# Performance work log

Hardware: AMD Instinct MI355X
Metric: run time of the kernel (lower is better)

The kernel has to match this reference:

```python
import math
import jax, jax.numpy as jnp
import numpy as np

G, NP, L = 256, 24, 3            # graphs, atoms per graph, GPS layers
C, TDIM, NFREQ, NT = 256, 256, 10, 100
EDIM = NFREQ * 2 * 3 + 9         # SinusoidsEmbedding.dim + lattice_input_dim = 69
N = G * NP                       # 6144 nodes
H = 4                            # attention heads


def _silu(x):
    return x * jax.nn.sigmoid(x)


def _bn(x, g, b):
    # BatchNorm1d, training-mode batch statistics (biased var), eps=1e-5
    m = x.mean(0)
    v = ((x - m) ** 2).mean(0)
    return (x - m) * jax.lax.rsqrt(v + 1e-5) * g + b


def _forward(t, frac_coords, lattice, type_emb, node_align_W, node_align_b,
             gine_edge_W, gine_edge_b, gine_W1, gine_b1, gine_W2, gine_b2,
             attn_in_W, attn_in_b, attn_out_W, attn_out_b,
             mlp_W1, mlp_b1, mlp_W2, mlp_b2,
             bn1_g, bn1_b, bn2_g, bn2_b, bn3_g, bn3_b, ln_g, ln_b,
             tro_W1, tro_b1, tro_W2, tro_b2,
             lat_W1, lat_b1, lat_W2, lat_b2, lat_W3,
             fc_W1, fc_b1, fc_W2, fc_b2, fc_W3,
             atom_types, node2graph, edge_src, edge_dst):
    # sinusoidal time embedding [G, TDIM], repeated per node
    half = TDIM // 2
    tf = jnp.exp(jnp.arange(half, dtype=jnp.float32) * (-math.log(10000.0) / (half - 1)))
    te = t[:, None] * tf[None, :]
    te = jnp.concatenate([jnp.sin(te), jnp.cos(te)], -1)
    time_emb = jnp.repeat(te, NP, axis=0)                      # [N, TDIM]
    x = jnp.concatenate([type_emb[atom_types], time_emb], 1) @ node_align_W + node_align_b

    # edge features: sinusoids of periodic frac diff + per-graph lattice
    fd = (frac_coords[edge_dst] - frac_coords[edge_src]) % 1.0  # [E,3]
    sf = 2.0 * math.pi * jnp.arange(NFREQ, dtype=jnp.float32)
    emb = (fd[..., None] * sf).reshape(-1, 3 * NFREQ)
    eattr = jnp.concatenate([jnp.sin(emb), jnp.cos(emb), lattice[node2graph[edge_src]]], 1)

    scale = 1.0 / math.sqrt(C // H)
    for l in range(L):
        # --- GINEConv: gather -> relu(x_j + edge_emb) -> scatter-add -> MLP ---
        eemb = eattr @ gine_edge_W[l] + gine_edge_b[l]          # [E, C]
        msg = jax.nn.relu(x[edge_src] + eemb)
        aggr = jax.ops.segment_sum(msg, edge_dst, num_segments=N)
        z = x + aggr                                            # (1+eps)*x, eps=0
        z = _silu(z @ gine_W1[l] + gine_b1[l]) @ gine_W2[l] + gine_b2[l]
        h1 = _bn(z + x, bn1_g[l], bn1_b[l])
        # --- dense-batched multihead self-attention (all graphs have NP nodes) ---
        xd = x.reshape(G, NP, C)
        qkv = xd @ attn_in_W[l] + attn_in_b[l]
        q, k, v = jnp.split(qkv, 3, axis=-1)
        q = q.reshape(G, NP, H, C // H).transpose(0, 2, 1, 3)
        k = k.reshape(G, NP, H, C // H).transpose(0, 2, 1, 3)
        v = v.reshape(G, NP, H, C // H).transpose(0, 2, 1, 3)
        a = jax.nn.softmax(jnp.einsum('ghqd,ghkd->ghqk', q, k) * scale, axis=-1)
        o = jnp.einsum('ghqk,ghkd->ghqd', a, v).transpose(0, 2, 1, 3).reshape(G, NP, C)
        o = (o @ attn_out_W[l] + attn_out_b[l]).reshape(N, C)
        h2 = _bn(o + x, bn2_g[l], bn2_b[l])
        # --- combine + MLP (GPSConv default: ReLU, dropout=0) ---
        out = h1 + h2
        out = out + jax.nn.relu(out @ mlp_W1[l] + mlp_b1[l]) @ mlp_W2[l] + mlp_b2[l]
        x = _bn(out, bn3_g[l], bn3_b[l])

    # final LayerNorm over feature dim
    m = x.mean(-1, keepdims=True)
    v = ((x - m) ** 2).mean(-1, keepdims=True)
    hn = (x - m) * jax.lax.rsqrt(v + 1e-5) * ln_g + ln_b

    # scatter-mean graph pooling
    cnt = jax.ops.segment_sum(jnp.ones((N, 1), hn.dtype), node2graph, num_segments=G)
    gf = jax.ops.segment_sum(hn, node2graph, num_segments=G) / cnt

    types_pred = _silu(hn @ tro_W1 + tro_b1) @ tro_W2 + tro_b2
    lattice_pred = _silu(_silu(gf @ lat_W1 + lat_b1) @ lat_W2 + lat_b2) @ lat_W3
    frac_pred = _silu(_silu(hn @ fc_W1 + fc_b1) @ fc_W2 + fc_b2) @ fc_W3
    return types_pred, lattice_pred, frac_pred


def setup_inputs() -> dict:
    key = jax.random.key(0)
    ki = iter(jax.random.split(key, 40))

    def nrm(shape, s=0.02):
        return jax.random.normal(next(ki), shape, jnp.float32) * s

    # block-diagonal fully-connected edges, dense_to_sparse row-major order
    g = np.repeat(np.arange(G), NP * NP)
    i = np.tile(np.repeat(np.arange(NP), NP), G)
    j = np.tile(np.tile(np.arange(NP), NP), G)
    inp = {
        "t": jax.random.uniform(next(ki), (G,), jnp.float32),
        "frac_coords": jax.random.uniform(next(ki), (N, 3), jnp.float32),
        "lattice": nrm((G, 9), 1.0),
        "type_emb": nrm((NT, C)),
        "node_align_W": nrm((C + TDIM, C)), "node_align_b": jnp.zeros((C,), jnp.float32),
        "gine_edge_W": nrm((L, EDIM, C)), "gine_edge_b": jnp.zeros((L, C), jnp.float32),
        "gine_W1": nrm((L, C, C)), "gine_b1": jnp.zeros((L, C), jnp.float32),
        "gine_W2": nrm((L, C, C)), "gine_b2": jnp.zeros((L, C), jnp.float32),
        "attn_in_W": nrm((L, C, 3 * C)), "attn_in_b": jnp.zeros((L, 3 * C), jnp.float32),
        "attn_out_W": nrm((L, C, C)), "attn_out_b": jnp.zeros((L, C), jnp.float32),
        "mlp_W1": nrm((L, C, 2 * C)), "mlp_b1": jnp.zeros((L, 2 * C), jnp.float32),
        "mlp_W2": nrm((L, 2 * C, C)), "mlp_b2": jnp.zeros((L, C), jnp.float32),
        "bn1_g": jnp.ones((L, C), jnp.float32), "bn1_b": jnp.zeros((L, C), jnp.float32),
        "bn2_g": jnp.ones((L, C), jnp.float32), "bn2_b": jnp.zeros((L, C), jnp.float32),
        "bn3_g": jnp.ones((L, C), jnp.float32), "bn3_b": jnp.zeros((L, C), jnp.float32),
        "ln_g": jnp.ones((C,), jnp.float32), "ln_b": jnp.zeros((C,), jnp.float32),
        "tro_W1": nrm((C, C // 2)), "tro_b1": jnp.zeros((C // 2,), jnp.float32),
        "tro_W2": nrm((C // 2, NT)), "tro_b2": jnp.zeros((NT,), jnp.float32),
        "lat_W1": nrm((C, C // 2)), "lat_b1": jnp.zeros((C // 2,), jnp.float32),
        "lat_W2": nrm((C // 2, C // 4)), "lat_b2": jnp.zeros((C // 4,), jnp.float32),
        "lat_W3": nrm((C // 4, 9)),
        "fc_W1": nrm((C, C // 2)), "fc_b1": jnp.zeros((C // 2,), jnp.float32),
        "fc_W2": nrm((C // 2, C // 4)), "fc_b2": jnp.zeros((C // 4,), jnp.float32),
        "fc_W3": nrm((C // 4, 3)),
        "atom_types": jax.random.randint(next(ki), (N,), 0, NT, jnp.int32),
        "node2graph": jnp.asarray(np.repeat(np.arange(G), NP), jnp.int32),
        "edge_src": jnp.asarray(g * NP + i, jnp.int32),
        "edge_dst": jnp.asarray(g * NP + j, jnp.int32),
    }
    return inp


def reference(t, frac_coords, lattice, type_emb, node_align_W, node_align_b,
              gine_edge_W, gine_edge_b, gine_W1, gine_b1, gine_W2, gine_b2,
              attn_in_W, attn_in_b, attn_out_W, attn_out_b,
              mlp_W1, mlp_b1, mlp_W2, mlp_b2,
              bn1_g, bn1_b, bn2_g, bn2_b, bn3_g, bn3_b, ln_g, ln_b,
              tro_W1, tro_b1, tro_W2, tro_b2,
              lat_W1, lat_b1, lat_W2, lat_b2, lat_W3,
              fc_W1, fc_b1, fc_W2, fc_b2, fc_W3,
              atom_types, node2graph, edge_src, edge_dst):
    return _forward(t, frac_coords, lattice, type_emb, node_align_W, node_align_b,
                    gine_edge_W, gine_edge_b, gine_W1, gine_b1, gine_W2, gine_b2,
                    attn_in_W, attn_in_b, attn_out_W, attn_out_b,
                    mlp_W1, mlp_b1, mlp_W2, mlp_b2,
                    bn1_g, bn1_b, bn2_g, bn2_b, bn3_g, bn3_b, ln_g, ln_b,
                    tro_W1, tro_b1, tro_W2, tro_b2,
                    lat_W1, lat_b1, lat_W2, lat_b2, lat_W3,
                    fc_W1, fc_b1, fc_W2, fc_b2, fc_W3,
                    atom_types, node2graph, edge_src, edge_dst)
```

## Files before the change

kernel.cpp:

```cpp
#include <hip/hip_runtime.h>
#include <hip/hip_bf16.h>
#include <math.h>

#define GG 256
#define NP 24
#define LL 3
#define CC 256
#define NN (GG*NP)
#define HH 4
#define DH 64

typedef __hip_bfloat16 bf;
typedef __attribute__((ext_vector_type(8))) short bfrag;
typedef __attribute__((ext_vector_type(4))) float ffrag;

__device__ __forceinline__ short pk(float x) {
    union { bf h; short s; } u; u.h = __float2bfloat16(x); return u.s;
}
__device__ __forceinline__ float b2f_s(short x) {
    union { short s; bf h; } u; u.s = x; return __bfloat162float(u.h);
}

typedef __attribute__((address_space(1))) const void gv_t;
typedef __attribute__((address_space(3))) void lv_t;

__global__ void detect_int_k(const unsigned int* __restrict__ at, int* flags) {
    __shared__ int ok;
    if (threadIdx.x == 0) ok = 1;
    __syncthreads();
    if (at[2 * threadIdx.x + 1] != 0u) ok = 0;
    __syncthreads();
    if (threadIdx.x == 0) flags[0] = ok;
}

__global__ void signal_k(float* out, int n, float val) {
    int i = blockIdx.x * 256 + threadIdx.x;
    if (i < n) out[i] = val;
}

struct TArgs {
    const float* src[9];
    long dstOff[9];
    int K[9], N[9], L[9];
    int blk0[10];
};
__global__ void transp_all(TArgs a, bf* __restrict__ wt) {
    int bid = blockIdx.x;
    int s = 0;
    while (s < 8 && bid >= a.blk0[s + 1]) ++s;
    long idx = (long)(bid - a.blk0[s]) * 256 + threadIdx.x;
    int KN = a.K[s] * a.N[s];
    long sz = (long)KN * a.L[s];
    if (idx >= sz) return;
    int l = (int)(idx / KN);
    int rem = (int)(idx % KN);
    int k = rem / a.N[s], n = rem % a.N[s];
    wt[a.dstOff[s] + (long)l * KN + (long)n * a.K[s] + k] =
        __float2bfloat16(a.src[s][idx]);
}

#define ETAB_ELEMS (GG * 24 * 24 * 64)
__global__ void prep_gewtab(const float* __restrict__ geW, short* __restrict__ wh,
                            short* __restrict__ wl, const float* __restrict__ frac,
                            short* __restrict__ eh, short* __restrict__ el) {
    int bid = blockIdx.x;
    if (bid < 192) {
        int idx = bid * 256 + threadIdx.x;
        if (idx >= 49152) return;
        int k = idx & 63;
        int n = (idx >> 6) & 127;
        int half = (idx >> 13) & 1;
        int l = idx >> 14;
        float v = (k < 60) ? geW[(long)l * 69 * 256 + (long)k * 256 + half * 128 + n] : 0.f;
        short hi = pk(v);
        short lo = pk(v - b2f_s(hi));
        wh[idx] = hi;
        wl[idx] = lo;
    } else {
        int idx = (bid - 192) * 256 + threadIdx.x;
        if (idx >= ETAB_ELEMS) return;
        int k = idx & 63;
        int rem = idx >> 6;
        int i = rem % 24;
        int rem2 = rem / 24;
        int j = rem2 % 24;
        int g = rem2 / 24;
        float val = 0.f;
        if (k < 60) {
            int r = (k < 30) ? k : k - 30;
            int d = r / 10, f = r % 10;
            float fd = frac[g * 72 + j * 3 + d] - frac[g * 72 + i * 3 + d];
            fd -= floorf(fd);
            float ang = 6.283185307179586f * (float)f * fd;
            val = (k < 30) ? sinf(ang) : cosf(ang);
        }
        short hi = pk(val);
        eh[idx] = hi;
        el[idx] = pk(val - b2f_s(hi));
    }
}

__global__ void build_A(const float* __restrict__ t, const float* __restrict__ type_emb,
                        const unsigned int* __restrict__ atoms,
                        float* __restrict__ A, const int* __restrict__ flags) {
    int i64 = flags[0];
    int idx = blockIdx.x * 256 + threadIdx.x;
    if (idx >= NN * 512) return;
    int n = idx >> 9;
    int k = idx & 511;
    if (k < 256) {
        int a = i64 ? (int)atoms[2 * n] : (int)atoms[n];
        A[idx] = type_emb[(long)a * CC + k];
    } else {
        int d = k - 256;
        int g = n / NP;
        float tv = t[g];
        int dd = (d < 128) ? d : d - 128;
        float tf = expf(dd * (-9.210340371976184f / 127.0f));
        float ang = tv * tf;
        A[idx] = (d < 128) ? sinf(ang) : cosf(ang);
    }
}

__global__ __launch_bounds__(256) void gemm_mfma(
        const float* __restrict__ A, const bf* __restrict__ Wt,
        const float* __restrict__ bias, const float* __restrict__ bias2,
        const float* __restrict__ res,
        float* __restrict__ C, int M, int K, int N, int act) {
    __shared__ __align__(16) short As[2][32 * 72];
    __shared__ __align__(16) short Bs[2][2][64 * 32];
    int tid = threadIdx.x;
    int lane = tid & 63, w = tid >> 6;
    int wm = w & 1, wn = w >> 1;
    int m0 = blockIdx.x * 32, n0 = blockIdx.y * 64;
    ffrag acc[2] = {};
    int sa_m = tid >> 3, sa_k = (tid & 7) << 3;
    int fr_row = lane & 15, quad = lane >> 4, fr_k = quad << 3;
    int brow = w * 16 + (lane >> 2);
    int bko = (lane & 3) << 3;
    const short* wsrc = (const short*)Wt + (long)(n0 + brow) * K + bko;

    {
        const float* Ap = A + (long)(m0 + sa_m) * K + sa_k;
        float4 a1 = *(const float4*)Ap;
        float4 a2 = *(const float4*)(Ap + 4);
        __builtin_amdgcn_global_load_lds((gv_t*)(wsrc), (lv_t*)(&Bs[0][0][w * 512]), 16, 0, 0);
        __builtin_amdgcn_global_load_lds((gv_t*)(wsrc + 32), (lv_t*)(&Bs[0][1][w * 512]), 16, 0, 0);
        short* ap = &As[0][sa_m * 72 + sa_k];
        ap[0] = pk(a1.x); ap[1] = pk(a1.y); ap[2] = pk(a1.z); ap[3] = pk(a1.w);
        ap[4] = pk(a2.x); ap[5] = pk(a2.y); ap[6] = pk(a2.z); ap[7] = pk(a2.w);
    }
    __syncthreads();

    int nk = K >> 6;
    int cur = 0;
    for (int i = 0; i < nk; ++i) {
        float4 a1n, a2n;
        bool more = (i + 1) < nk;
        if (more) {
            int kn = (i + 1) << 6;
            __builtin_amdgcn_global_load_lds((gv_t*)(wsrc + kn),
                (lv_t*)(&Bs[cur ^ 1][0][w * 512]), 16, 0, 0);
            __builtin_amdgcn_global_load_lds((gv_t*)(wsrc + kn + 32),
                (lv_t*)(&Bs[cur ^ 1][1][w * 512]), 16, 0, 0);
            const float* Ap = A + (long)(m0 + sa_m) * K + kn + sa_k;
            a1n = *(const float4*)Ap;
            a2n = *(const float4*)(Ap + 4);
        }
        bfrag af0  = *(const bfrag*)(&As[cur][(wm * 16 + fr_row) * 72 + fr_k]);
        bfrag af1  = *(const bfrag*)(&As[cur][(wm * 16 + fr_row) * 72 + 32 + fr_k]);
        bfrag bg00 = *(const bfrag*)(&Bs[cur][0][(wn * 32 + fr_row) * 32 + fr_k]);
        bfrag bg01 = *(const bfrag*)(&Bs[cur][0][(wn * 32 + 16 + fr_row) * 32 + fr_k]);
        bfrag bg10 = *(const bfrag*)(&Bs[cur][1][(wn * 32 + fr_row) * 32 + fr_k]);
        bfrag bg11 = *(const bfrag*)(&Bs[cur][1][(wn * 32 + 16 + fr_row) * 32 + fr_k]);
        acc[0] = __builtin_amdgcn_mfma_f32_16x16x32_bf16(af0, bg00, acc[0], 0, 0, 0);
        acc[1] = __builtin_amdgcn_mfma_f32_16x16x32_bf16(af0, bg01, acc[1], 0, 0, 0);
        acc[0] = __builtin_amdgcn_mfma_f32_16x16x32_bf16(af1, bg10, acc[0], 0, 0, 0);
        acc[1] = __builtin_amdgcn_mfma_f32_16x16x32_bf16(af1, bg11, acc[1], 0, 0, 0);
        if (more) {
            short* ap = &As[cur ^ 1][sa_m * 72 + sa_k];
            ap[0] = pk(a1n.x); ap[1] = pk(a1n.y); ap[2] = pk(a1n.z); ap[3] = pk(a1n.w);
            ap[4] = pk(a2n.x); ap[5] = pk(a2n.y); ap[6] = pk(a2n.z); ap[7] = pk(a2n.w);
        }
        __syncthreads();
        cur ^= 1;
    }

    int mbase = (lane >> 4) << 2;
#pragma unroll
    for (int nt = 0; nt < 2; ++nt) {
        int n = n0 + wn * 32 + nt * 16 + (lane & 15);
        float bv = bias ? ((bias2 && n >= 128) ? bias2[n - 128] : bias[n]) : 0.f;
#pragma unroll
        for (int r = 0; r < 4; ++r) {
            int m = m0 + wm * 16 + mbase + r;
            float v = acc[nt][r] + bv;
            if (act == 1) v = fmaxf(v, 0.f);
            else if (act == 2) v = v / (1.f + expf(-v));
            if (res) v += res[(long)m * N + n];
            C[(long)m * N + n] = v;
        }
    }
}

__global__ __launch_bounds__(256) void gemm_k(
        const float* __restrict__ A, int lda, const float* __restrict__ W,
        const float* __restrict__ bias, const float* __restrict__ res,
        float* __restrict__ Cf, int M, int K, int Nc, int act) {
    __shared__ __align__(16) float Asf[32][64];
    __shared__ __align__(16) float Bsf[32][64];
    int tid = threadIdx.x;
    int tx = tid & 15, ty = tid >> 4;
    int m0 = blockIdx.x * 64, n0 = blockIdx.y * 64;
    float acc[4][4] = {{0.f}};
    int am = tid >> 2;
    int ak = (tid & 3) << 3;
    int bk = tid >> 4;
    int bn = (tid & 15) << 2;

    for (int k0 = 0; k0 < K; k0 += 32) {
        const float* Ap = A + (long)(m0 + am) * lda + k0 + ak;
        float4 a1 = *(const float4*)Ap;
        float4 a2 = *(const float4*)(Ap + 4);
        float w1[4], w2[4];
#pragma unroll
        for (int u = 0; u < 4; ++u) {
            int n = n0 + bn + u;
            w1[u] = (n < Nc) ? W[(long)(k0 + bk) * Nc + n] : 0.f;
            w2[u] = (n < Nc) ? W[(long)(k0 + bk + 16) * Nc + n] : 0.f;
        }
        __syncthreads();
        Asf[ak + 0][am] = a1.x; Asf[ak + 1][am] = a1.y;
        Asf[ak + 2][am] = a1.z; Asf[ak + 3][am] = a1.w;
        Asf[ak + 4][am] = a2.x; Asf[ak + 5][am] = a2.y;
        Asf[ak + 6][am] = a2.z; Asf[ak + 7][am] = a2.w;
#pragma unroll
        for (int u = 0; u < 4; ++u) {
            Bsf[bk][bn + u] = w1[u];
            Bsf[bk + 16][bn + u] = w2[u];
        }
        __syncthreads();
#pragma unroll
        for (int k = 0; k < 32; ++k) {
            float4 a = *(const float4*)(&Asf[k][ty << 2]);
            float4 b = *(const float4*)(&Bsf[k][tx << 2]);
            acc[0][0] += a.x * b.x; acc[0][1] += a.x * b.y; acc[0][2] += a.x * b.z; acc[0][3] += a.x * b.w;
            acc[1][0] += a.y * b.x; acc[1][1] += a.y * b.y; acc[1][2] += a.y * b.z; acc[1][3] += a.y * b.w;
            acc[2][0] += a.z * b.x; acc[2][1] += a.z * b.y; acc[2][2] += a.z * b.z; acc[2][3] += a.z * b.w;
            acc[3][0] += a.w * b.x; acc[3][1] += a.w * b.y; acc[3][2] += a.w * b.z; acc[3][3] += a.w * b.w;
        }
    }
#pragma unroll
    for (int i = 0; i < 4; ++i) {
        int m = m0 + (ty << 2) + i;
#pragma unroll
        for (int j = 0; j < 4; ++j) {
            int n = n0 + (tx << 2) + j;
            if (n >= Nc) continue;
            float v = acc[i][j];
            if (bias) v += bias[n];
            if (act == 1) v = fmaxf(v, 0.f);
            else if (act == 2) v = v / (1.f + expf(-v));
            if (res) v += res[(long)m * Nc + n];
            Cf[(long)m * Nc + n] = v;
        }
    }
}

#define MF(a, b, c) c = __builtin_amdgcn_mfma_f32_16x16x32_bf16(a, b, c, 0, 0, 0)

__device__ __forceinline__ void stage_etile(const short* __restrict__ ej_h,
                                            const short* __restrict__ ej_l,
                                            short* lds_base, int w, int lane) {
    {
        int c = w;
        const short* src = (c < 3) ? (ej_h + c * 512) : (ej_l + (c - 3) * 512);
        int doff = (c < 3) ? c * 512 : 2048 + (c - 3) * 512;
        __builtin_amdgcn_global_load_lds((gv_t*)(src + lane * 8),
                                         (lv_t*)(lds_base + doff), 16, 0, 0);
    }
    if (w < 2) {
        int c = w + 4;
        const short* src = ej_l + (c - 3) * 512;
        int doff = 2048 + (c - 3) * 512;
        __builtin_amdgcn_global_load_lds((gv_t*)(src + lane * 8),
                                         (lv_t*)(lds_base + doff), 16, 0, 0);
    }
}

__global__ __launch_bounds__(256, 4) void gine4(
        const float* __restrict__ x,
        const float* __restrict__ lattice, const float* __restrict__ geW,
        const float* __restrict__ geb, const short* __restrict__ gewt_h,
        const short* __restrict__ gewt_l, const short* __restrict__ et_h,
        const short* __restrict__ et_l, float* __restrict__ z, int l) {
    __shared__ __align__(16) float xls[24 * 132];
    __shared__ float basel[128];
    __shared__ __align__(16) short ebuf[8192];

    int tid = threadIdx.x;
    int lane = tid & 63, w = tid >> 6, quad = lane >> 4, l16 = lane & 15;
    int g = blockIdx.x >> 2;
    int half = (blockIdx.x >> 1) & 1;
    int jh = blockIdx.x & 1;

    {
        const float4* xg = (const float4*)x;
        for (int idx = tid; idx < 768; idx += 256) {
            int i = idx >> 5, c4 = idx & 31;
            ((float4*)(xls + i * 132))[c4] =
                xg[((long)(g * NP + i) * CC + half * 128) / 4 + c4];
        }
    }
    if (tid < 128) {
        int cg = half * 128 + tid;
        float bv = geb[(long)l * CC + cg];
#pragma unroll
        for (int q = 0; q < 9; ++q)
            bv += lattice[(long)g * 9 + q] * geW[(long)l * 69 * 256 + (long)(60 + q) * 256 + cg];
        basel[tid] = bv;
    }

    bfrag bh00, bh01, bh10, bh11, bl00, bl01, bl10, bl11;
    {
        long base = (long)(l * 2 + half) * 8192;
        int nrow0 = w * 32 + l16;
        int nrow1 = w * 32 + 16 + l16;
        const short* p0h = gewt_h + base + nrow0 * 64 + quad * 8;
        const short* p1h = gewt_h + base + nrow1 * 64 + quad * 8;
        const short* p0l = gewt_l + base + nrow0 * 64 + quad * 8;
        const short* p1l = gewt_l + base + nrow1 * 64 + quad * 8;
        bh00 = *(const bfrag*)(p0h);      bh01 = *(const bfrag*)(p0h + 32);
        bh10 = *(const bfrag*)(p1h);      bh11 = *(const bfrag*)(p1h + 32);
        bl00 = *(const bfrag*)(p0l);      bl01 = *(const bfrag*)(p0l + 32);
        bl10 = *(const bfrag*)(p1l);      bl11 = *(const bfrag*)(p1l + 32);
    }

    const short* ehg = et_h + (long)g * (24 * 24 * 64);
    const short* elg = et_l + (long)g * (24 * 24 * 64);
    int j0 = jh * 12;

    stage_etile(ehg + (long)j0 * 1536, elg + (long)j0 * 1536, ebuf, w, lane);
    __syncthreads();

    float bse0 = basel[w * 32 + l16];
    float bse1 = basel[w * 32 + 16 + l16];

    int cur = 0;
    for (int jc = 0; jc < 12; ++jc) {
        int j = j0 + jc;
        if (jc < 11) {
            stage_etile(ehg + (long)(j + 1) * 1536, elg + (long)(j + 1) * 1536,
                        ebuf + (cur ^ 1) * 4096, w, lane);
        }

        const short* eb = ebuf + cur * 4096;
        int r0 = l16 * 64 + quad * 8;
        int r1 = (16 + l16) * 64 + quad * 8;
        bfrag ah00 = *(const bfrag*)(eb + r0);
        bfrag ah01 = *(const bfrag*)(eb + r0 + 32);
        bfrag ah10 = *(const bfrag*)(eb + r1);
        bfrag ah11 = *(const bfrag*)(eb + r1 + 32);
        bfrag al00 = *(const bfrag*)(eb + 2048 + r0);
        bfrag al01 = *(const bfrag*)(eb + 2048 + r0 + 32);
        bfrag al10 = *(const bfrag*)(eb + 2048 + r1);
        bfrag al11 = *(const bfrag*)(eb + 2048 + r1 + 32);

        ffrag a00 = {}, a01 = {}, a10 = {}, a11 = {};
        MF(ah00, bh00, a00); MF(ah00, bl00, a00); MF(al00, bh00, a00);
        MF(ah00, bh10, a01); MF(ah00, bl10, a01); MF(al00, bh10, a01);
        MF(ah01, bh01, a00); MF(ah01, bl01, a00); MF(al01, bh01, a00);
        MF(ah01, bh11, a01); MF(ah01, bl11, a01); MF(al01, bh11, a01);
        MF(ah10, bh00, a10); MF(ah10, bl00, a10); MF(al10, bh00, a10);
        MF(ah10, bh10, a11); MF(ah10, bl10, a11); MF(al10, bh10, a11);
        MF(ah11, bh01, a10); MF(ah11, bl01, a10); MF(al11, bh01, a10);
        MF(ah11, bh11, a11); MF(ah11, bl11, a11); MF(al11, bh11, a11);

#pragma unroll
        for (int nt = 0; nt < 2; ++nt) {
            int cl = w * 32 + nt * 16 + l16;
            float bse = nt ? bse1 : bse0;
            ffrag am0 = nt ? a01 : a00;
            ffrag am1 = nt ? a11 : a10;
            float part = 0.f;
            {
                int ibase = quad * 4;
#pragma unroll
                for (int r = 0; r < 4; ++r) {
                    float xv = xls[(ibase + r) * 132 + cl];
                    part += fmaxf(xv + bse + am0[r], 0.f);
                }
            }
            if (quad < 2) {
                int ibase = 16 + quad * 4;
#pragma unroll
                for (int r = 0; r < 4; ++r) {
                    float xv = xls[(ibase + r) * 132 + cl];
                    part += fmaxf(xv + bse + am1[r], 0.f);
                }
            }
            part += __shfl_xor(part, 16);
            part += __shfl_xor(part, 32);
            if (lane < 16)
                z[(long)(g * NP + j) * CC + half * 128 + cl] = xls[j * 132 + cl] + part;
        }
        __syncthreads();
        cur ^= 1;
    }
}

__global__ void bn_stats1(const float* __restrict__ in, float* __restrict__ part) {
    int c = threadIdx.x, b = blockIdx.x;
    float s = 0.f, q = 0.f;
    for (int r = 0; r < 64; ++r) {
        float v = in[(long)(b * 64 + r) * CC + c];
        s += v; q += v * v;
    }
    part[b * 512 + c] = s;
    part[b * 512 + 256 + c] = q;
}
__global__ __launch_bounds__(256) void bn_apply2(
        const float* __restrict__ in, const float* __restrict__ part,
        const float* __restrict__ gma, const float* __restrict__ bta,
        const float* __restrict__ add, float* __restrict__ out) {
    int c = threadIdx.x;
    float s = 0.f, q = 0.f;
    for (int b = 0; b < 96; ++b) { s += part[b * 512 + c]; q += part[b * 512 + 256 + c]; }
    float m = s / (float)NN;
    float var = q / (float)NN - m * m;
    float stats_c = m;
    float stats_rs = rsqrtf(var + 1e-5f);
    float gc = gma[c], bc = bta[c];
    for (int r = blockIdx.x; r < NN; r += 768) {
        long idx = (long)r * CC + c;
        float v = (in[idx] - stats_c) * stats_rs * gc + bc;
        if (add) v += add[idx];
        out[idx] = v;
    }
}

__global__ __launch_bounds__(256, 2) void attn2(const float* __restrict__ qkv,
                                                float* __restrict__ o) {
    __shared__ __align__(16) float Kl[24 * 4 * 68];
    __shared__ __align__(16) float Vl[24 * 4 * 68];
    __shared__ float S[4 * 24 * 25];
    int tid = threadIdx.x, g = blockIdx.x;

    const float4* qkv4 = (const float4*)(qkv + (long)g * NP * 768);
    for (int idx = tid; idx < 24 * 128; idx += 256) {
        int row = idx >> 7;
        int c4 = idx & 127;
        int isV = c4 >> 6;
        int cc = c4 & 63;
        int h = cc >> 4, d4 = cc & 15;
        float4 val = qkv4[row * 192 + 64 + c4];
        float* dst = (isV ? Vl : Kl) + (row * 4 + h) * 68 + d4 * 4;
        *(float4*)dst = val;
    }
    __syncthreads();

    if (tid < 96) {
        int h = tid & 3, i = tid >> 2;
        const float4* qp = (const float4*)(qkv + ((long)(g * NP + i)) * 768 + h * 64);
        float4 q[16];
#pragma unroll
        for (int k = 0; k < 16; ++k) q[k] = qp[k];
        float sc[24];
        float mx = -1e30f;
        for (int j = 0; j < 24; ++j) {
            const float4* kp = (const float4*)(Kl + (j * 4 + h) * 68);
            float da = 0.f, db = 0.f;
#pragma unroll
            for (int k = 0; k < 16; k += 2) {
                float4 kv = kp[k];
                da += q[k].x * kv.x; da += q[k].y * kv.y;
                da += q[k].z * kv.z; da += q[k].w * kv.w;
                float4 kv2 = kp[k + 1];
                db += q[k + 1].x * kv2.x; db += q[k + 1].y * kv2.y;
                db += q[k + 1].z * kv2.z; db += q[k + 1].w * kv2.w;
            }
            float s = (da + db) * 0.125f;
            sc[j] = s;
            mx = fmaxf(mx, s);
        }
        float sum = 0.f;
#pragma unroll
        for (int j = 0; j < 24; ++j) { float p = expf(sc[j] - mx); sc[j] = p; sum += p; }
        float inv = 1.f / sum;
#pragma unroll
        for (int j = 0; j < 24; ++j) S[(h * 24 + i) * 25 + j] = sc[j] * inv;
    }
    __syncthreads();

    int h = tid >> 6, d = tid & 63;
    for (int i = 0; i < 24; ++i) {
        const float* Sp = S + (h * 24 + i) * 25;
        float a0 = 0.f, a1 = 0.f;
#pragma unroll
        for (int j = 0; j < 24; j += 2) {
            a0 += Sp[j] * Vl[(j * 4 + h) * 68 + d];
            a1 += Sp[j + 1] * Vl[((j + 1) * 4 + h) * 68 + d];
        }
        o[(long)(g * NP + i) * CC + h * 64 + d] = a0 + a1;
    }
}

__global__ __launch_bounds__(256) void ln_kernel(const float* __restrict__ x,
        const float* __restrict__ gma, const float* __restrict__ bta,
        float* __restrict__ out) {
    __shared__ float red[256];
    int n = blockIdx.x, c = threadIdx.x;
    float v = x[(long)n * CC + c];
    red[c] = v;
    __syncthreads();
    for (int s = 128; s > 0; s >>= 1) { if (c < s) red[c] += red[c + s]; __syncthreads(); }
    float m = red[0] * (1.f / 256.f);
    __syncthreads();
    float dv = v - m;
    red[c] = dv * dv;
    __syncthreads();
    for (int s = 128; s > 0; s >>= 1) { if (c < s) red[c] += red[c + s]; __syncthreads(); }
    float var = red[0] * (1.f / 256.f);
    out[(long)n * CC + c] = dv * rsqrtf(var + 1e-5f) * gma[c] + bta[c];
}

__global__ __launch_bounds__(256) void lat_head(
        const float* __restrict__ hn, const float* __restrict__ W1,
        const float* __restrict__ b1, const float* __restrict__ W2,
        const float* __restrict__ b2, const float* __restrict__ W3,
        float* __restrict__ out) {
    __shared__ float gfl[256];
    __shared__ float h1[128];
    __shared__ float h2[64];
    int g = blockIdx.x, t = threadIdx.x;
    {
        float s = 0.f;
        for (int j = 0; j < NP; ++j) s += hn[(long)(g * NP + j) * CC + t];
        gfl[t] = s * (1.f / 24.f);
    }
    __syncthreads();
    if (t < 128) {
        float acc = 0.f;
        for (int k = 0; k < 256; ++k) acc += gfl[k] * W1[k * 128 + t];
        float v = acc;
        v += b1[t];
        v = v / (1.f + expf(-v));
        h1[t] = v;
    }
    __syncthreads();
    if (t < 64) {
        float acc = 0.f;
        for (int k = 0; k < 128; ++k) acc += h1[k] * W2[k * 64 + t];
        float v = acc;
        v += b2[t];
        v = v / (1.f + expf(-v));
        h2[t] = v;
    }
    __syncthreads();
    if (t < 9) {
        float acc = 0.f;
        for (int k = 0; k < 64; ++k) acc += h2[k] * W3[k * 9 + t];
        out[(long)g * 9 + t] = acc;
    }
}

static void gemm(hipStream_t st, const float* A, int lda, const float* W,
                 const float* bias, const float* res, float* Cf,
                 int M, int K, int Nc, int act) {
    dim3 grid(M / 64, (Nc + 63) / 64);
    gemm_k<<<grid, 256, 0, st>>>(A, lda, W, bias, res, Cf, M, K, Nc, act);
}

static void gemmM(hipStream_t st, const float* A, const bf* Wt, const float* bias,
                  const float* bias2, const float* res, float* Cf,
                  int M, int K, int N, int act) {
    dim3 grid(M / 32, N / 64);
    gemm_mfma<<<grid, 256, 0, st>>>(A, Wt, bias, bias2, res, Cf, M, K, N, act);
}

static void run_bn(hipStream_t st, const float* in, float* part,
                   const float* g_, const float* b_, const float* add, float* out) {
    bn_stats1<<<96, 256, 0, st>>>(in, part);
    bn_apply2<<<768, 256, 0, st>>>(in, part, g_, b_, add, out);
}

extern "C" void kernel_launch(void* const* d_in, const int* in_sizes, int n_in,
                              void* d_out, int out_size, void* d_ws, size_t ws_size,
                              hipStream_t stream) {
    float* out = (float*)d_out;
    int sigN = out_size < 256 ? out_size : 256;

    static const int EXP_SIZES[46] = {
        256, 18432, 2304, 25600, 131072, 256, 52992, 768, 196608, 768,
        196608, 768, 589824, 2304, 196608, 768, 393216, 1536, 393216, 768,
        768, 768, 768, 768, 768, 768, 256, 256, 32768, 128,
        12800, 100, 32768, 128, 8192, 64, 576, 32768, 128, 8192,
        64, 192, 6144, 6144, 147456, 147456 };
    if (n_in != 46) { signal_k<<<1, 256, 0, stream>>>(out, sigN, 3000.f + 8.f * n_in); return; }
    for (int i = 0; i < 46; ++i)
        if (in_sizes[i] != EXP_SIZES[i]) { signal_k<<<1, 256, 0, stream>>>(out, sigN, 512.f + 8.f * i); return; }
    if (out_size != NN * 100 + GG * 9 + NN * 3) { signal_k<<<1, 256, 0, stream>>>(out, sigN, 7777.f); return; }

    char* base = (char*)d_ws;
    int* flags = (int*)base;
    float* f32a = (float*)(base + 256);
    float* x  = f32a;
    float* s1 = x  + (size_t)NN * 256;
    float* s2 = s1 + (size_t)NN * 256;
    float* big = s2 + (size_t)NN * 256;
    float* s3 = big + (size_t)NN * 512;
    float* part = big + (size_t)NN * 768;
    float* stats = part + 96 * 512;
    float* gf  = stats + 512;
    float* l1b = gf + GG * 256;
    float* l2b = l1b + GG * 128;
    bf* wt = (bf*)(l2b + GG * 64);
    const long O_NA = 0, O_G1 = 131072, O_G2 = 327680, O_AI = 524288,
               O_AO = 1114112, O_M1 = 1310720, O_M2 = 1703936,
               O_TRO = 2097152, O_FC = 2129920, WT_TOT = 2162688;
    short* gewt_h = (short*)(wt + WT_TOT);
    short* gewt_l = gewt_h + 49152;
    short* et_h = gewt_l + 49152;
    short* et_l = et_h + (ETAB_ELEMS + 1024);
    size_t REQ = 256 + ((size_t)NN * 1536 + 96 * 512 + 512 + GG * 448) * 4
               + WT_TOT * 2 + 49152 * 2 * 2
               + ((size_t)ETAB_ELEMS + 1024) * 2 * 2;
    if (ws_size < REQ) { signal_k<<<1, 256, 0, stream>>>(out, sigN, 9999.f); return; }

    const float* t       = (const float*)d_in[0];
    const float* frac    = (const float*)d_in[1];
    const float* lattice = (const float*)d_in[2];
    const float* type_emb = (const float*)d_in[3];

    detect_int_k<<<1, 256, 0, stream>>>((const unsigned int*)d_in[42], flags);

    {
        TArgs ta;
        const int srcIdx[9] = {4, 8, 10, 12, 14, 16, 18, 28, 37};
        const long dof[9]  = {O_NA, O_G1, O_G2, O_AI, O_AO, O_M1, O_M2, O_TRO, O_FC};
        const int Ks[9] = {512, 256, 256, 256, 256, 256, 512, 256, 256};
        const int Ns[9] = {256, 256, 256, 768, 256, 512, 256, 128, 128};
        const int Ls[9] = {1, 3, 3, 3, 3, 3, 3, 1, 1};
        int blk = 0;
        for (int s = 0; s < 9; ++s) {
            ta.src[s] = (const float*)d_in[srcIdx[s]];
            ta.dstOff[s] = dof[s];
            ta.K[s] = Ks[s]; ta.N[s] = Ns[s]; ta.L[s] = Ls[s];
            ta.blk0[s] = blk;
            blk += (Ks[s] * Ns[s] * Ls[s] + 255) / 256;
        }
        ta.blk0[9] = blk;
        transp_all<<<blk, 256, 0, stream>>>(ta, wt);
    }
    prep_gewtab<<<192 + (ETAB_ELEMS + 255) / 256, 256, 0, stream>>>(
        (const float*)d_in[6], gewt_h, gewt_l, frac, et_h, et_l);

    build_A<<<(NN * 512 + 255) / 256, 256, 0, stream>>>(t, type_emb,
        (const unsigned int*)d_in[42], big, flags);
    gemmM(stream, big, wt + O_NA, (const float*)d_in[5], nullptr, nullptr, x, NN, 512, 256, 0);

    for (int l = 0; l < LL; ++l) {
        gine4<<<GG * 4, 256, 0, stream>>>(x, lattice,
            (const float*)d_in[6], (const float*)d_in[7], gewt_h, gewt_l,
            et_h, et_l, s1, l);
        gemmM(stream, s1, wt + O_G1 + (long)l * 65536, (const float*)d_in[9]  + l * 256, nullptr, nullptr, s2, NN, 256, 256, 2);
        gemmM(stream, s2, wt + O_G2 + (long)l * 65536, (const float*)d_in[11] + l * 256, nullptr, x, s3, NN, 256, 256, 0);
        run_bn(stream, s3, part, (const float*)d_in[20] + l * 256, (const float*)d_in[21] + l * 256, nullptr, s2);
        gemmM(stream, x, wt + O_AI + (long)l * 196608, (const float*)d_in[13] + l * 768, nullptr, nullptr, big, NN, 256, 768, 0);
        attn2<<<GG, 256, 0, stream>>>(big, s1);
        gemmM(stream, s1, wt + O_AO + (long)l * 65536, (const float*)d_in[15] + l * 256, nullptr, x, s3, NN, 256, 256, 0);
        run_bn(stream, s3, part, (const float*)d_in[22] + l * 256, (const float*)d_in[23] + l * 256, s2, s1);
        gemmM(stream, s1, wt + O_M1 + (long)l * 131072, (const float*)d_in[17] + l * 512, nullptr, nullptr, big, NN, 256, 512, 1);
        gemmM(stream, big, wt + O_M2 + (long)l * 131072, (const float*)d_in[19] + l * 256, nullptr, s1, s3, NN, 512, 256, 0);
        run_bn(stream, s3, part, (const float*)d_in[24] + l * 256, (const float*)d_in[25] + l * 256, nullptr, x);
    }

    ln_kernel<<<NN, 256, 0, stream>>>(x, (const float*)d_in[26], (const float*)d_in[27], s1);

    gemmM(stream, s1, wt + O_TRO, (const float*)d_in[29], (const float*)d_in[38],
          nullptr, s2, NN, 256, 256, 2);
    gemm(stream, s2, 256, (const float*)d_in[30], (const float*)d_in[31], nullptr, out, NN, 128, 100, 0);
    lat_head<<<GG, 256, 0, stream>>>(s1, (const float*)d_in[32], (const float*)d_in[33],
        (const float*)d_in[34], (const float*)d_in[35], (const float*)d_in[36],
        out + (size_t)NN * 100);
    gemm(stream, s2 + 128, 256, (const float*)d_in[39], (const float*)d_in[40], nullptr, s3, NN, 128, 64, 2);
    gemm(stream, s3, 64, (const float*)d_in[41], nullptr, nullptr, out + (size_t)NN * 100 + GG * 9, NN, 64, 3, 0);
}
```

Before: 712.5 us.

## Fuse back-to-back MLP GEMM pairs into one kernel keeping intermediate in LDS

Adds a gemm2_fused kernel that computes two chained GEMMs per 16-row strip. The bf16 intermediate activation stays in shared memory and is never written to global memory. It replaces the GINE MLP pair and the feed-forward MLP pair in every layer, removing the global round trip of the intermediate and one launch per pair. In exchange, each block handles only 16 rows and reloads every weight tile, so weight traffic per row grows. Each 64-wide output tile runs a serial K loop with a sync per step, which may limit MFMA utilisation.

```diff
diff --git a/kernel.cpp b/kernel.cpp
--- a/kernel.cpp
+++ b/kernel.cpp
@@ -203,6 +203,122 @@
     }
 }
 
+template<int N1>
+__global__ __launch_bounds__(256) void gemm2_fused(
+        const float* __restrict__ A, const bf* __restrict__ Wt1,
+        const float* __restrict__ bias1, int act1,
+        const bf* __restrict__ Wt2, const float* __restrict__ bias2,
+        const float* __restrict__ res, float* __restrict__ C) {
+    constexpr int PITCH = N1 + 8;
+    __shared__ __align__(16) short Astrip[16 * 264];
+    __shared__ __align__(16) short Strip[16 * PITCH];
+    __shared__ __align__(16) short Bs[2][2][64 * 32];
+    int tid = threadIdx.x;
+    int lane = tid & 63, w = tid >> 6;
+    int m0 = blockIdx.x * 16;
+    int fr_row = lane & 15, quad = lane >> 4, fr_k = quad << 3;
+    int brow = w * 16 + (lane >> 2);
+    int bko = (lane & 3) << 3;
+    int mbase = quad << 2;
+    int l15 = lane & 15;
+
+    {
+        int row = tid >> 4, seg = (tid & 15) << 4;
+        const float* Ap = A + (long)(m0 + row) * 256 + seg;
+        short* dst = &Astrip[row * 264 + seg];
+#pragma unroll
+        for (int u = 0; u < 16; u += 4) {
+            float4 a = *(const float4*)(Ap + u);
+            dst[u + 0] = pk(a.x); dst[u + 1] = pk(a.y);
+            dst[u + 2] = pk(a.z); dst[u + 3] = pk(a.w);
+        }
+    }
+
+    for (int t4 = 0; t4 < N1 / 64; ++t4) {
+        int n0 = t4 * 64;
+        const short* wsrc = (const short*)Wt1 + (long)(n0 + brow) * 256 + bko;
+        __builtin_amdgcn_global_load_lds((gv_t*)(wsrc), (lv_t*)(&Bs[0][0][w * 512]), 16, 0, 0);
+        __builtin_amdgcn_global_load_lds((gv_t*)(wsrc + 32), (lv_t*)(&Bs[0][1][w * 512]), 16, 0, 0);
+        __syncthreads();
+        ffrag acc = {};
+        int cur = 0;
+        for (int i = 0; i < 4; ++i) {
+            bool more = (i + 1) < 4;
+            if (more) {
+                int kn = (i + 1) << 6;
+                __builtin_amdgcn_global_load_lds((gv_t*)(wsrc + kn),
+                    (lv_t*)(&Bs[cur ^ 1][0][w * 512]), 16, 0, 0);
+                __builtin_amdgcn_global_load_lds((gv_t*)(wsrc + kn + 32),
+                    (lv_t*)(&Bs[cur ^ 1][1][w * 512]), 16, 0, 0);
+            }
+            int k0 = i << 6;
+            const short* arow = &Astrip[fr_row * 264 + k0];
+            bfrag af0 = *(const bfrag*)(arow + fr_k);
+            bfrag af1 = *(const bfrag*)(arow + 32 + fr_k);
+            bfrag bg0 = *(const bfrag*)(&Bs[cur][0][(w * 16 + fr_row) * 32 + fr_k]);
+            bfrag bg1 = *(const bfrag*)(&Bs[cur][1][(w * 16 + fr_row) * 32 + fr_k]);
+            acc = __builtin_amdgcn_mfma_f32_16x16x32_bf16(af0, bg0, acc, 0, 0, 0);
+            acc = __builtin_amdgcn_mfma_f32_16x16x32_bf16(af1, bg1, acc, 0, 0, 0);
+            __syncthreads();
+            cur ^= 1;
+        }
+        {
+            int n = n0 + w * 16 + l15;
+            float bv = bias1[n];
+#pragma unroll
+            for (int r = 0; r < 4; ++r) {
+                int ml = mbase + r;
+                float v = acc[r] + bv;
+                if (act1 == 1) v = fmaxf(v, 0.f);
+                else if (act1 == 2) v = v / (1.f + expf(-v));
+                Strip[ml * PITCH + n] = pk(v);
+            }
+        }
+    }
+
+    constexpr int NK2 = N1 >> 6;
+    for (int t4 = 0; t4 < 4; ++t4) {
+        int n0 = t4 * 64;
+        const short* wsrc = (const short*)Wt2 + (long)(n0 + brow) * N1 + bko;
+        __builtin_amdgcn_global_load_lds((gv_t*)(wsrc), (lv_t*)(&Bs[0][0][w * 512]), 16, 0, 0);
+        __builtin_amdgcn_global_load_lds((gv_t*)(wsrc + 32), (lv_t*)(&Bs[0][1][w * 512]), 16, 0, 0);
+        __syncthreads();
+        ffrag acc = {};
+        int cur = 0;
+        for (int i = 0; i < NK2; ++i) {
+            bool more = (i + 1) < NK2;
+            if (more) {
+                int kn = (i + 1) << 6;
+                __builtin_amdgcn_global_load_lds((gv_t*)(wsrc + kn),
+                    (lv_t*)(&Bs[cur ^ 1][0][w * 512]), 16, 0, 0);
+                __builtin_amdgcn_global_load_lds((gv_t*)(wsrc + kn + 32),
+                    (lv_t*)(&Bs[cur ^ 1][1][w * 512]), 16, 0, 0);
+            }
+            int k0 = i << 6;
+            const short* arow = &Strip[fr_row * PITCH + k0];
+            bfrag af0 = *(const bfrag*)(arow + fr_k);
+            bfrag af1 = *(const bfrag*)(arow + 32 + fr_k);
+            bfrag bg0 = *(const bfrag*)(&Bs[cur][0][(w * 16 + fr_row) * 32 + fr_k]);
+            bfrag bg1 = *(const bfrag*)(&Bs[cur][1][(w * 16 + fr_row) * 32 + fr_k]);
+            acc = __builtin_amdgcn_mfma_f32_16x16x32_bf16(af0, bg0, acc, 0, 0, 0);
+            acc = __builtin_amdgcn_mfma_f32_16x16x32_bf16(af1, bg1, acc, 0, 0, 0);
+            __syncthreads();
+            cur ^= 1;
+        }
+        {
+            int n = n0 + w * 16 + l15;
+            float bv = bias2[n];
+#pragma unroll
+            for (int r = 0; r < 4; ++r) {
+                int m = m0 + mbase + r;
+                float v = acc[r] + bv;
+                v += res[(long)m * 256 + n];
+                C[(long)m * 256 + n] = v;
+            }
+        }
+    }
+}
+
 __global__ __launch_bounds__(256) void gemm_k(
         const float* __restrict__ A, int lda, const float* __restrict__ W,
         const float* __restrict__ bias, const float* __restrict__ res,
@@ -663,15 +779,17 @@
         gine4<<<GG * 4, 256, 0, stream>>>(x, lattice,
             (const float*)d_in[6], (const float*)d_in[7], gewt_h, gewt_l,
             et_h, et_l, s1, l);
-        gemmM(stream, s1, wt + O_G1 + (long)l * 65536, (const float*)d_in[9]  + l * 256, nullptr, nullptr, s2, NN, 256, 256, 2);
-        gemmM(stream, s2, wt + O_G2 + (long)l * 65536, (const float*)d_in[11] + l * 256, nullptr, x, s3, NN, 256, 256, 0);
+        gemm2_fused<256><<<NN / 16, 256, 0, stream>>>(s1,
+            wt + O_G1 + (long)l * 65536, (const float*)d_in[9] + l * 256, 2,
+            wt + O_G2 + (long)l * 65536, (const float*)d_in[11] + l * 256, x, s3);
         run_bn(stream, s3, part, (const float*)d_in[20] + l * 256, (const float*)d_in[21] + l * 256, nullptr, s2);
         gemmM(stream, x, wt + O_AI + (long)l * 196608, (const float*)d_in[13] + l * 768, nullptr, nullptr, big, NN, 256, 768, 0);
         attn2<<<GG, 256, 0, stream>>>(big, s1);
         gemmM(stream, s1, wt + O_AO + (long)l * 65536, (const float*)d_in[15] + l * 256, nullptr, x, s3, NN, 256, 256, 0);
         run_bn(stream, s3, part, (const float*)d_in[22] + l * 256, (const float*)d_in[23] + l * 256, s2, s1);
-        gemmM(stream, s1, wt + O_M1 + (long)l * 131072, (const float*)d_in[17] + l * 512, nullptr, nullptr, big, NN, 256, 512, 1);
-        gemmM(stream, big, wt + O_M2 + (long)l * 131072, (const float*)d_in[19] + l * 256, nullptr, s1, s3, NN, 512, 256, 0);
+        gemm2_fused<512><<<NN / 16, 256, 0, stream>>>(s1,
+            wt + O_M1 + (long)l * 131072, (const float*)d_in[17] + l * 512, 1,
+            wt + O_M2 + (long)l * 131072, (const float*)d_in[19] + l * 256, s1, s3);
         run_bn(stream, s3, part, (const float*)d_in[24] + l * 256, (const float*)d_in[25] + l * 256, nullptr, x);
     }
 
```

After: 758.4 us. 6.4% more time.
